# Kernel optimization log

Measured on AMD Instinct MI355X. Metric: run time of the kernel, lower is better.

## Reference

```python
import jax, jax.numpy as jnp
import numpy as np

B, N, M, V = 256, 16354, 512, 4096
S = round((N - 2) / (M - 1))  # = 32, stride of conv1d_st1_2 and conv1d_xt


def conv1d(x, w, b, stride, padding):
    # x: [B, L], w: [1, 1, K], b: [1] -> [B, L_out]
    y = jax.lax.conv_general_dilated(x[:, None, :], w, (stride,), [(padding, padding)])
    return y[:, 0, :] + b


def setup_inputs() -> dict:
    key = jax.random.key(0)
    ks = jax.random.split(key, 25)
    rn = lambda k, shape, s=0.1: (jax.random.normal(k, shape, jnp.float32) * s)
    return {
        "st1": jax.random.normal(ks[0], (B, N), jnp.float32),
        "ht1": jax.random.normal(ks[1], (B, M), jnp.float32),
        "zt": jax.random.normal(ks[2], (B, N - 1), jnp.float32),
        "da_t": jax.random.randint(ks[3], (B,), 0, N),
        "w_st1": rn(ks[4], (1, 1, 5)), "b_st1": rn(ks[5], (1,)),
        "w_st12": rn(ks[6], (1, 1, 2)), "b_st12": rn(ks[7], (1,)),
        "w_mt1": rn(ks[8], (1, 1, 3)), "b_mt1": rn(ks[9], (1,)),
        "w_xt": rn(ks[10], (1, 1, 2)), "b_xt": rn(ks[11], (1,)),
        "W_ih": rn(ks[12], (3 * M, M)), "W_hh": rn(ks[13], (3 * M, M)),
        "b_ih": rn(ks[14], (3 * M,)), "b_hh": rn(ks[15], (3 * M,)),
        "w_lht": rn(ks[16], (1, M)), "b_lht": rn(ks[17], (1,)),
        "w_lct": rn(ks[18], (1, M + 1)), "b_lct": rn(ks[19], (1,)),
        "emb": rn(ks[20], (V, N), 1.0),
    }


def reference(st1, ht1, zt, da_t, w_st1, b_st1, w_st12, b_st12, w_mt1, b_mt1,
              w_xt, b_xt, W_ih, W_hh, b_ih, b_hh, w_lht, b_lht, w_lct, b_lct, emb):
    da_f = da_t.astype(st1.dtype)[:, None]  # [B, 1]
    # Mt1_0: two chained 1-channel convs st1 [B,N] -> [B,M]
    Mt1_0 = conv1d(conv1d(st1, w_st1, b_st1, 1, 2), w_st12, b_st12, S, 0)
    Mt1 = jnp.concatenate([Mt1_0, ht1], axis=1)           # [B, 2M]
    Ht1 = conv1d(jax.nn.relu(Mt1), w_mt1, b_mt1, 2, 1)    # [B, M] (GRU h0)
    xt = conv1d(jnp.concatenate([zt, da_f], axis=1), w_xt, b_xt, S, 0)  # [B, M]
    # single-step GRU (torch gate math)
    gi = xt @ W_ih.T + b_ih
    gh = Ht1 @ W_hh.T + b_hh
    ir, iz, inn = jnp.split(gi, 3, axis=1)
    hr, hz, hn = jnp.split(gh, 3, axis=1)
    r = jax.nn.sigmoid(ir + hr)
    z = jax.nn.sigmoid(iz + hz)
    n_ = jnp.tanh(inn + r * hn)
    ht = (1.0 - z) * n_ + z * Ht1                         # [B, M]
    # index into frozen embedding: ((V-1)*sigmoid(linear(ht))).long()
    it = jnp.floor((V - 1) * jax.nn.sigmoid(ht @ w_lht.T + b_lht)[:, 0]).astype(jnp.int32)
    srt = jax.lax.stop_gradient(emb[it])                  # [B, N], no_grad in original
    ct = jax.nn.sigmoid(jnp.concatenate([ht, da_f], axis=1) @ w_lct.T + b_lct)[:, 0]  # [B]
    # vectorized per-row shift + zero-pad + scale (replaces the Python batch loop)
    idx = da_t[:, None] + jnp.arange(N)[None, :]          # [B, N]
    valid = idx < N
    shifted = jnp.where(valid, jnp.take_along_axis(st1, jnp.minimum(idx, N - 1), axis=1), 0.0)
    st = shifted * ct[:, None] + srt                      # [B, N]
    return st, ht
```

## Files before the change

kernel.cpp:

```cpp
#include <hip/hip_runtime.h>
#include <cstdint>
#include <cstddef>

constexpr int B_  = 256;
constexpr int N_  = 16354;
constexpr int M_  = 512;
constexpr int V_  = 4096;
constexpr int S_  = 32;
constexpr int G3  = 1536;

__global__ __launch_bounds__(512) void k_front(
    const float* __restrict__ st1, const float* __restrict__ ht1,
    const float* __restrict__ zt, const int* __restrict__ da_t,
    const float* __restrict__ w_st1, const float* __restrict__ b_st1,
    const float* __restrict__ w_st12, const float* __restrict__ b_st12,
    const float* __restrict__ w_mt1, const float* __restrict__ b_mt1,
    const float* __restrict__ w_xt, const float* __restrict__ b_xt,
    float* __restrict__ xt_out, float* __restrict__ ht1c_out)
{
    __shared__ float sm[2 * M_];
    const int b = blockIdx.x;
    const int j = threadIdx.x;

    const float* srow = st1 + (size_t)b * N_;

    const float w0 = w_st1[0], w1 = w_st1[1], w2 = w_st1[2], w3 = w_st1[3], w4 = w_st1[4];
    const float bs = b_st1[0];

    const int p = S_ * j;
    float x[6];
    if (j > 0 && j < M_ - 1) {
        const float2 a = *(const float2*)(srow + p - 2);
        const float2 c = *(const float2*)(srow + p);
        const float2 d = *(const float2*)(srow + p + 2);
        x[0] = a.x; x[1] = a.y; x[2] = c.x; x[3] = c.y; x[4] = d.x; x[5] = d.y;
    } else {
        #pragma unroll
        for (int k = 0; k < 6; ++k) {
            int ix = p - 2 + k;
            x[k] = (ix >= 0 && ix < N_) ? srow[ix] : 0.0f;
        }
    }
    float y0 = bs;
    y0 = fmaf(x[0], w0, y0); y0 = fmaf(x[1], w1, y0); y0 = fmaf(x[2], w2, y0);
    y0 = fmaf(x[3], w3, y0); y0 = fmaf(x[4], w4, y0);
    float y1 = bs;
    y1 = fmaf(x[1], w0, y1); y1 = fmaf(x[2], w1, y1); y1 = fmaf(x[3], w2, y1);
    y1 = fmaf(x[4], w3, y1); y1 = fmaf(x[5], w4, y1);

    const float m0 = fmaf(y0, w_st12[0], fmaf(y1, w_st12[1], b_st12[0]));
    sm[j]      = m0;
    sm[M_ + j] = ht1[(size_t)b * M_ + j];

    const float daf = (float)da_t[b];
    const float* zrow = zt + (size_t)b * (N_ - 1);
    const float u0 = zrow[S_ * j];
    const float u1 = (j == M_ - 1) ? daf : zrow[S_ * j + 1];
    xt_out[(size_t)b * M_ + j] = fmaf(u0, w_xt[0], fmaf(u1, w_xt[1], b_xt[0]));

    __syncthreads();

    const int q = 2 * j;
    float vm1 = 0.0f, v0, vp1 = 0.0f;
    if (q - 1 >= 0) { float t = sm[q - 1]; vm1 = t > 0.0f ? t : 0.0f; }
    { float t = sm[q]; v0 = t > 0.0f ? t : 0.0f; }
    if (q + 1 < 2 * M_) { float t = sm[q + 1]; vp1 = t > 0.0f ? t : 0.0f; }
    const float hv = fmaf(vm1, w_mt1[0], fmaf(v0, w_mt1[1], fmaf(vp1, w_mt1[2], b_mt1[0])));
    ht1c_out[(size_t)b * M_ + j] = hv;
}

constexpr int BMg = 256;
constexpr int BNg = 16;
constexpr int BKg = 32;
constexpr int PA  = 36;
constexpr size_t GPART = (size_t)B_ * G3;

__global__ __launch_bounds__(256, 3) void k_gemm(
    const float* __restrict__ xt, const float* __restrict__ Ht1c,
    const float* __restrict__ W_ih, const float* __restrict__ W_hh,
    float* __restrict__ g, int kper)
{
    __shared__ __align__(16) float As[BMg][PA];
    __shared__ __align__(16) float Ws[BNg][PA];

    const int t = threadIdx.x;
    const int z = blockIdx.y;
    int n0 = blockIdx.x * BNg;

    const float* A;
    const float* W;
    float* out;
    if (n0 < G3) { A = xt;   W = W_ih; out = g + (size_t)(2 * z + 0) * GPART; }
    else         { A = Ht1c; W = W_hh; out = g + (size_t)(2 * z + 1) * GPART; n0 -= G3; }

    const int srow = t >> 3;
    const int sk4  = (t & 7) * 4;

    const int fm = t & 31;
    const int fn = (t >> 5) * 2;

    float acc[8][2];
    #pragma unroll
    for (int i = 0; i < 8; ++i) { acc[i][0] = 0.0f; acc[i][1] = 0.0f; }

    const int kbeg = z * kper;
    const int kend = kbeg + kper;

    for (int k0 = kbeg; k0 < kend; k0 += BKg) {
        #pragma unroll
        for (int i = 0; i < 8; ++i) {
            const float4 v = *(const float4*)(A + (size_t)(srow + 32 * i) * M_ + k0 + sk4);
            *(float4*)&As[srow + 32 * i][sk4] = v;
        }
        if (t < 128) {
            const float4 v = *(const float4*)(W + (size_t)(n0 + (t >> 3)) * M_ + k0 + sk4);
            *(float4*)&Ws[t >> 3][sk4] = v;
        }
        __syncthreads();

        #pragma unroll
        for (int k4 = 0; k4 < 8; ++k4) {
            const float4 w0 = *(const float4*)&Ws[fn][4 * k4];
            const float4 w1 = *(const float4*)&Ws[fn + 1][4 * k4];
            #pragma unroll
            for (int i = 0; i < 8; ++i) {
                const float4 a = *(const float4*)&As[fm + 32 * i][4 * k4];
                acc[i][0] = fmaf(a.x, w0.x, acc[i][0]);
                acc[i][0] = fmaf(a.y, w0.y, acc[i][0]);
                acc[i][0] = fmaf(a.z, w0.z, acc[i][0]);
                acc[i][0] = fmaf(a.w, w0.w, acc[i][0]);
                acc[i][1] = fmaf(a.x, w1.x, acc[i][1]);
                acc[i][1] = fmaf(a.y, w1.y, acc[i][1]);
                acc[i][1] = fmaf(a.z, w1.z, acc[i][1]);
                acc[i][1] = fmaf(a.w, w1.w, acc[i][1]);
            }
        }
        __syncthreads();
    }

    #pragma unroll
    for (int i = 0; i < 8; ++i) {
        float2 o; o.x = acc[i][0]; o.y = acc[i][1];
        *(float2*)&out[(size_t)(fm + 32 * i) * G3 + n0 + fn] = o;
    }
}

__global__ __launch_bounds__(1024) void k_tail(
    const float* __restrict__ g, int zs,
    const float* __restrict__ b_ih, const float* __restrict__ b_hh,
    const float* __restrict__ Ht1c, const int* __restrict__ da_t,
    const float* __restrict__ w_lht, const float* __restrict__ b_lht,
    const float* __restrict__ w_lct, const float* __restrict__ b_lct,
    const float* __restrict__ st1, const float* __restrict__ emb,
    float* __restrict__ ht_out, float* __restrict__ st_out)
{
    __shared__ float red1[8], red2[8];
    __shared__ float s_ct;
    __shared__ int   s_it;

    const int b = blockIdx.x;
    const int o = threadIdx.x;
    const int da = da_t[b];

    if (o < M_) {
        float ir = 0.f, iz = 0.f, inn = 0.f, hr = 0.f, hz = 0.f, hn = 0.f;
        for (int zz = 0; zz < zs; ++zz) {
            const float* gib = g + (size_t)(2 * zz + 0) * GPART + (size_t)b * G3;
            const float* ghb = g + (size_t)(2 * zz + 1) * GPART + (size_t)b * G3;
            ir  += gib[o];
            iz  += gib[M_ + o];
            inn += gib[2 * M_ + o];
            hr  += ghb[o];
            hz  += ghb[M_ + o];
            hn  += ghb[2 * M_ + o];
        }
        ir  += b_ih[o];
        iz  += b_ih[M_ + o];
        inn += b_ih[2 * M_ + o];
        hr  += b_hh[o];
        hz  += b_hh[M_ + o];
        hn  += b_hh[2 * M_ + o];

        const float r  = 1.0f / (1.0f + expf(-(ir + hr)));
        const float z  = 1.0f / (1.0f + expf(-(iz + hz)));
        const float n_ = tanhf(fmaf(r, hn, inn));
        const float hprev = Ht1c[(size_t)b * M_ + o];
        const float h = (1.0f - z) * n_ + z * hprev;

        ht_out[(size_t)b * M_ + o] = h;

        float p1 = h * w_lht[o];
        float p2 = h * w_lct[o];
        #pragma unroll
        for (int off = 32; off > 0; off >>= 1) {
            p1 += __shfl_down(p1, off);
            p2 += __shfl_down(p2, off);
        }
        const int wid = o >> 6, lane = o & 63;
        if (lane == 0) { red1[wid] = p1; red2[wid] = p2; }
    }
    __syncthreads();
    if (o == 0) {
        float s1 = 0.0f, s2 = 0.0f;
        #pragma unroll
        for (int i = 0; i < 8; ++i) { s1 += red1[i]; s2 += red2[i]; }
        const float a1 = s1 + b_lht[0];
        const float sg1 = 1.0f / (1.0f + expf(-a1));
        s_it = (int)floorf((float)(V_ - 1) * sg1);

        const float daf = (float)da;
        const float a2 = s2 + daf * w_lct[M_] + b_lct[0];
        s_ct = 1.0f / (1.0f + expf(-a2));
    }
    __syncthreads();

    const int   it = s_it;
    const float ct = s_ct;

    const float* er = emb + (size_t)it * N_;
    const float* sr = st1 + (size_t)b * N_;
    float* orow     = st_out + (size_t)b * N_;

    const float2* er2 = (const float2*)er;
    float2* orow2     = (float2*)orow;
    constexpr int H = N_ / 2;

    if ((da & 1) == 0) {
        for (int k = o; k < H; k += 1024) {
            const int i = 2 * k;
            const int idx = da + i;
            float2 sv;
            if (idx + 1 < N_)      sv = *(const float2*)(sr + idx);
            else if (idx < N_)     { sv.x = sr[idx]; sv.y = 0.0f; }
            else                   { sv.x = 0.0f; sv.y = 0.0f; }
            const float2 e = er2[k];
            float2 ov;
            ov.x = fmaf(sv.x, ct, e.x);
            ov.y = fmaf(sv.y, ct, e.y);
            orow2[k] = ov;
        }
    } else {
        for (int k = o; k < H; k += 1024) {
            const int i = 2 * k;
            const int idx = da + i;
            float2 sv;
            sv.x = (idx < N_)     ? sr[idx]     : 0.0f;
            sv.y = (idx + 1 < N_) ? sr[idx + 1] : 0.0f;
            const float2 e = er2[k];
            float2 ov;
            ov.x = fmaf(sv.x, ct, e.x);
            ov.y = fmaf(sv.y, ct, e.y);
            orow2[k] = ov;
        }
    }
}

extern "C" void kernel_launch(void* const* d_in, const int* in_sizes, int n_in,
                              void* d_out, int out_size, void* d_ws, size_t ws_size,
                              hipStream_t stream)
{
    const float* st1   = (const float*)d_in[0];
    const float* ht1   = (const float*)d_in[1];
    const float* zt    = (const float*)d_in[2];
    const int*   da_t  = (const int*)d_in[3];
    const float* w_st1 = (const float*)d_in[4];
    const float* b_st1 = (const float*)d_in[5];
    const float* w_st12= (const float*)d_in[6];
    const float* b_st12= (const float*)d_in[7];
    const float* w_mt1 = (const float*)d_in[8];
    const float* b_mt1 = (const float*)d_in[9];
    const float* w_xt  = (const float*)d_in[10];
    const float* b_xt  = (const float*)d_in[11];
    const float* W_ih  = (const float*)d_in[12];
    const float* W_hh  = (const float*)d_in[13];
    const float* b_ih  = (const float*)d_in[14];
    const float* b_hh  = (const float*)d_in[15];
    const float* w_lht = (const float*)d_in[16];
    const float* b_lht = (const float*)d_in[17];
    const float* w_lct = (const float*)d_in[18];
    const float* b_lct = (const float*)d_in[19];
    const float* emb   = (const float*)d_in[20];

    float* st_out = (float*)d_out;
    float* ht_out = (float*)d_out + (size_t)B_ * N_;

    float* ws   = (float*)d_ws;
    float* xt   = ws;
    float* Ht1c = xt + (size_t)B_ * M_;
    float* g    = Ht1c + (size_t)B_ * M_;

    const size_t base = 2 * (size_t)B_ * M_ * sizeof(float);
    int zs = 1;
    if (ws_size >= base + 8 * GPART * sizeof(float))      zs = 4;
    else if (ws_size >= base + 4 * GPART * sizeof(float)) zs = 2;
    const int kper = M_ / zs;

    k_front<<<dim3(B_), dim3(M_), 0, stream>>>(
        st1, ht1, zt, da_t, w_st1, b_st1, w_st12, b_st12,
        w_mt1, b_mt1, w_xt, b_xt, xt, Ht1c);

    k_gemm<<<dim3(2 * G3 / BNg, zs), dim3(256), 0, stream>>>(
        xt, Ht1c, W_ih, W_hh, g, kper);

    k_tail<<<dim3(B_), dim3(1024), 0, stream>>>(
        g, zs, b_ih, b_hh, Ht1c, da_t,
        w_lht, b_lht, w_lct, b_lct, st1, emb, ht_out, st_out);
}
```

Before: 43.57 us.

## Retile GRU GEMM into 64x96 register tiles with prefetch, split tail gate loads

The gate GEMM now uses 64x96 output tiles, with each thread computing a 4x6 register tile from k-major transposed shared memory. The next K slice is prefetched into registers while the current one is computed. The split-K factor is capped at 2, which gives fewer partial buffers for the tail to sum. The tail kernel now spreads the input-gate and hidden-gate partial loads across all 1024 threads and passes the hidden gates through shared memory. This raises arithmetic intensity per shared load but cuts grid size and occupancy.

```diff
diff --git a/kernel.cpp b/kernel.cpp
--- a/kernel.cpp
+++ b/kernel.cpp
@@ -69,22 +69,22 @@
     ht1c_out[(size_t)b * M_ + j] = hv;
 }
 
-constexpr int BMg = 256;
-constexpr int BNg = 16;
+constexpr int BMg = 64;
+constexpr int BNg = 96;
 constexpr int BKg = 32;
-constexpr int PA  = 36;
 constexpr size_t GPART = (size_t)B_ * G3;
 
-__global__ __launch_bounds__(256, 3) void k_gemm(
+__global__ __launch_bounds__(256) void k_gemm(
     const float* __restrict__ xt, const float* __restrict__ Ht1c,
     const float* __restrict__ W_ih, const float* __restrict__ W_hh,
     float* __restrict__ g, int kper)
 {
-    __shared__ __align__(16) float As[BMg][PA];
-    __shared__ __align__(16) float Ws[BNg][PA];
+    __shared__ __align__(16) float As[BKg][BMg + 4];
+    __shared__ __align__(16) float Ws[BKg][BNg + 4];
 
     const int t = threadIdx.x;
-    const int z = blockIdx.y;
+    const int z = blockIdx.z;
+    const int bm0 = blockIdx.y * BMg;
     int n0 = blockIdx.x * BNg;
 
     const float* A;
@@ -93,55 +93,85 @@
     if (n0 < G3) { A = xt;   W = W_ih; out = g + (size_t)(2 * z + 0) * GPART; }
     else         { A = Ht1c; W = W_hh; out = g + (size_t)(2 * z + 1) * GPART; n0 -= G3; }
 
-    const int srow = t >> 3;
-    const int sk4  = (t & 7) * 4;
-
-    const int fm = t & 31;
-    const int fn = (t >> 5) * 2;
-
-    float acc[8][2];
+    const int srow = t >> 2;
+    const int sk4  = (t & 3) * 4;
+    const int wrow = t >> 3;
+    const int wk4  = (t & 7) * 4;
+
+    const int tm = (t & 15) * 4;
+    const int tn = (t >> 4) * 6;
+
+    float acc[4][6];
     #pragma unroll
-    for (int i = 0; i < 8; ++i) { acc[i][0] = 0.0f; acc[i][1] = 0.0f; }
+    for (int i = 0; i < 4; ++i)
+        #pragma unroll
+        for (int jj = 0; jj < 6; ++jj) acc[i][jj] = 0.0f;
 
     const int kbeg = z * kper;
     const int kend = kbeg + kper;
 
+    const float* ap0 = A + (size_t)(bm0 + srow) * M_;
+    const float* wp0 = W + (size_t)(n0 + wrow) * M_;
+    const float* wp1 = W + (size_t)(n0 + wrow + 32) * M_;
+    const float* wp2 = W + (size_t)(n0 + wrow + 64) * M_;
+
+    float4 ra0, ra1, rw0, rw1, rw2;
+    {
+        ra0 = *(const float4*)(ap0 + kbeg + sk4);
+        ra1 = *(const float4*)(ap0 + kbeg + sk4 + 16);
+        rw0 = *(const float4*)(wp0 + kbeg + wk4);
+        rw1 = *(const float4*)(wp1 + kbeg + wk4);
+        rw2 = *(const float4*)(wp2 + kbeg + wk4);
+    }
+
     for (int k0 = kbeg; k0 < kend; k0 += BKg) {
-        #pragma unroll
-        for (int i = 0; i < 8; ++i) {
-            const float4 v = *(const float4*)(A + (size_t)(srow + 32 * i) * M_ + k0 + sk4);
-            *(float4*)&As[srow + 32 * i][sk4] = v;
-        }
-        if (t < 128) {
-            const float4 v = *(const float4*)(W + (size_t)(n0 + (t >> 3)) * M_ + k0 + sk4);
-            *(float4*)&Ws[t >> 3][sk4] = v;
-        }
         __syncthreads();
-
-        #pragma unroll
-        for (int k4 = 0; k4 < 8; ++k4) {
-            const float4 w0 = *(const float4*)&Ws[fn][4 * k4];
-            const float4 w1 = *(const float4*)&Ws[fn + 1][4 * k4];
+        As[sk4 + 0][srow] = ra0.x; As[sk4 + 1][srow] = ra0.y;
+        As[sk4 + 2][srow] = ra0.z; As[sk4 + 3][srow] = ra0.w;
+        As[16 + sk4 + 0][srow] = ra1.x; As[16 + sk4 + 1][srow] = ra1.y;
+        As[16 + sk4 + 2][srow] = ra1.z; As[16 + sk4 + 3][srow] = ra1.w;
+        Ws[wk4 + 0][wrow] = rw0.x; Ws[wk4 + 1][wrow] = rw0.y;
+        Ws[wk4 + 2][wrow] = rw0.z; Ws[wk4 + 3][wrow] = rw0.w;
+        Ws[wk4 + 0][wrow + 32] = rw1.x; Ws[wk4 + 1][wrow + 32] = rw1.y;
+        Ws[wk4 + 2][wrow + 32] = rw1.z; Ws[wk4 + 3][wrow + 32] = rw1.w;
+        Ws[wk4 + 0][wrow + 64] = rw2.x; Ws[wk4 + 1][wrow + 64] = rw2.y;
+        Ws[wk4 + 2][wrow + 64] = rw2.z; Ws[wk4 + 3][wrow + 64] = rw2.w;
+        __syncthreads();
+
+        const int kn = k0 + BKg;
+        if (kn < kend) {
+            ra0 = *(const float4*)(ap0 + kn + sk4);
+            ra1 = *(const float4*)(ap0 + kn + sk4 + 16);
+            rw0 = *(const float4*)(wp0 + kn + wk4);
+            rw1 = *(const float4*)(wp1 + kn + wk4);
+            rw2 = *(const float4*)(wp2 + kn + wk4);
+        }
+
+        #pragma unroll
+        for (int k = 0; k < BKg; ++k) {
+            const float4 a  = *(const float4*)&As[k][tm];
+            const float2 wa = *(const float2*)&Ws[k][tn];
+            const float2 wb = *(const float2*)&Ws[k][tn + 2];
+            const float2 wc = *(const float2*)&Ws[k][tn + 4];
+            const float av[4] = {a.x, a.y, a.z, a.w};
+            const float wv[6] = {wa.x, wa.y, wb.x, wb.y, wc.x, wc.y};
             #pragma unroll
-            for (int i = 0; i < 8; ++i) {
-                const float4 a = *(const float4*)&As[fm + 32 * i][4 * k4];
-                acc[i][0] = fmaf(a.x, w0.x, acc[i][0]);
-                acc[i][0] = fmaf(a.y, w0.y, acc[i][0]);
-                acc[i][0] = fmaf(a.z, w0.z, acc[i][0]);
-                acc[i][0] = fmaf(a.w, w0.w, acc[i][0]);
-                acc[i][1] = fmaf(a.x, w1.x, acc[i][1]);
-                acc[i][1] = fmaf(a.y, w1.y, acc[i][1]);
-                acc[i][1] = fmaf(a.z, w1.z, acc[i][1]);
-                acc[i][1] = fmaf(a.w, w1.w, acc[i][1]);
-            }
-        }
-        __syncthreads();
+            for (int i = 0; i < 4; ++i)
+                #pragma unroll
+                for (int jj = 0; jj < 6; ++jj)
+                    acc[i][jj] = fmaf(av[i], wv[jj], acc[i][jj]);
+        }
     }
 
     #pragma unroll
-    for (int i = 0; i < 8; ++i) {
-        float2 o; o.x = acc[i][0]; o.y = acc[i][1];
-        *(float2*)&out[(size_t)(fm + 32 * i) * G3 + n0 + fn] = o;
+    for (int i = 0; i < 4; ++i) {
+        float* orow = out + (size_t)(bm0 + tm + i) * G3 + n0 + tn;
+        float2 o0; o0.x = acc[i][0]; o0.y = acc[i][1];
+        float2 o1; o1.x = acc[i][2]; o1.y = acc[i][3];
+        float2 o2; o2.x = acc[i][4]; o2.y = acc[i][5];
+        *(float2*)(orow + 0) = o0;
+        *(float2*)(orow + 2) = o1;
+        *(float2*)(orow + 4) = o2;
     }
 }
 
@@ -154,6 +184,7 @@
     const float* __restrict__ st1, const float* __restrict__ emb,
     float* __restrict__ ht_out, float* __restrict__ st_out)
 {
+    __shared__ float shh[3][M_];
     __shared__ float red1[8], red2[8];
     __shared__ float s_ct;
     __shared__ int   s_it;
@@ -162,24 +193,34 @@
     const int o = threadIdx.x;
     const int da = da_t[b];
 
+    float ir = 0.f, iz = 0.f, inn = 0.f;
     if (o < M_) {
-        float ir = 0.f, iz = 0.f, inn = 0.f, hr = 0.f, hz = 0.f, hn = 0.f;
         for (int zz = 0; zz < zs; ++zz) {
             const float* gib = g + (size_t)(2 * zz + 0) * GPART + (size_t)b * G3;
-            const float* ghb = g + (size_t)(2 * zz + 1) * GPART + (size_t)b * G3;
             ir  += gib[o];
             iz  += gib[M_ + o];
             inn += gib[2 * M_ + o];
-            hr  += ghb[o];
-            hz  += ghb[M_ + o];
-            hn  += ghb[2 * M_ + o];
-        }
+        }
+    } else {
+        const int o2 = o - M_;
+        float hr = 0.f, hz = 0.f, hn = 0.f;
+        for (int zz = 0; zz < zs; ++zz) {
+            const float* ghb = g + (size_t)(2 * zz + 1) * GPART + (size_t)b * G3;
+            hr += ghb[o2];
+            hz += ghb[M_ + o2];
+            hn += ghb[2 * M_ + o2];
+        }
+        shh[0][o2] = hr; shh[1][o2] = hz; shh[2][o2] = hn;
+    }
+    __syncthreads();
+
+    if (o < M_) {
         ir  += b_ih[o];
         iz  += b_ih[M_ + o];
         inn += b_ih[2 * M_ + o];
-        hr  += b_hh[o];
-        hz  += b_hh[M_ + o];
-        hn  += b_hh[2 * M_ + o];
+        const float hr = shh[0][o] + b_hh[o];
+        const float hz = shh[1][o] + b_hh[M_ + o];
+        const float hn = shh[2][o] + b_hh[2 * M_ + o];
 
         const float r  = 1.0f / (1.0f + expf(-(ir + hr)));
         const float z  = 1.0f / (1.0f + expf(-(iz + hz)));
@@ -291,15 +332,14 @@
 
     const size_t base = 2 * (size_t)B_ * M_ * sizeof(float);
     int zs = 1;
-    if (ws_size >= base + 8 * GPART * sizeof(float))      zs = 4;
-    else if (ws_size >= base + 4 * GPART * sizeof(float)) zs = 2;
+    if (ws_size >= base + 4 * GPART * sizeof(float)) zs = 2;
     const int kper = M_ / zs;
 
     k_front<<<dim3(B_), dim3(M_), 0, stream>>>(
         st1, ht1, zt, da_t, w_st1, b_st1, w_st12, b_st12,
         w_mt1, b_mt1, w_xt, b_xt, xt, Ht1c);
 
-    k_gemm<<<dim3(2 * G3 / BNg, zs), dim3(256), 0, stream>>>(
+    k_gemm<<<dim3(2 * G3 / BNg, B_ / BMg, zs), dim3(256), 0, stream>>>(
         xt, Ht1c, W_ih, W_hh, g, kper);
 
     k_tail<<<dim3(B_), dim3(1024), 0, stream>>>(
```

Measured after the change: 43.87 us. No clear change (+0.7%).
